# Performance work log

Hardware: AMD Instinct MI355X
Metric: run time of the kernel (lower is better)

## Reference

```python
import jax, jax.numpy as jnp
import numpy as np

OUT_F, IN_F = 4096, 4096
GROUP = 128
NGROUPS = IN_F // GROUP  # 32


def setup_inputs() -> dict:
    key = jax.random.key(0)
    k1, k2, k3, k4 = jax.random.split(key, 4)
    x = jax.random.normal(k1, (4, 2048, IN_F), dtype=jnp.float32)
    # 4-bit codes stored as integers in [0, 16)
    compressed_weight = jax.random.randint(k2, (OUT_F, IN_F), 0, 16, dtype=jnp.int32)
    scale = jax.random.uniform(k3, (OUT_F, NGROUPS), dtype=jnp.float32)
    offset = jax.random.normal(k4, (OUT_F, NGROUPS), dtype=jnp.float32)
    return {"x": x, "compressed_weight": compressed_weight, "scale": scale, "offset": offset}


def reference(x, compressed_weight, scale, offset):
    # group-wise dequant: w[o, g, j] = code * scale[o, g] - offset[o, g]
    codes = compressed_weight.astype(scale.dtype).reshape(OUT_F, NGROUPS, GROUP)
    w = (codes * scale[..., None] - offset[..., None]).reshape(OUT_F, IN_F)
    # F.linear: x @ w.T  -> [B, S, OUT_F]
    return jnp.einsum('bsi,oi->bso', x, w.astype(x.dtype))
```

## Files before the change

### kernel.cpp

```cpp
#include <hip/hip_runtime.h>
#include <stdint.h>

#define OUT_F 4096
#define IN_F  4096
#define NGROUPS 32
#define BK 64
#define NT (IN_F / BK)

typedef __attribute__((ext_vector_type(4)))  float    f32x4;
typedef __attribute__((ext_vector_type(8)))  short    bf16x8;
typedef __attribute__((ext_vector_type(4)))  int      i32x4;
typedef __attribute__((ext_vector_type(4)))  uint32_t u32x4;

__device__ __forceinline__ ushort f2bf(float f) {
  union { float f; uint32_t u; } v; v.f = f;
  uint32_t r = v.u + 0x7FFFu + ((v.u >> 16) & 1u);
  return (ushort)(r >> 16);
}

__global__ void cvt_x_kernel(const float* __restrict__ x, ushort* __restrict__ xb, int n8) {
  int i = blockIdx.x * blockDim.x + threadIdx.x;
  if (i >= n8) return;
  const f32x4* xp = (const f32x4*)x;
  f32x4 a = xp[2 * i], b = xp[2 * i + 1];
  u32x4 o;
  o.x = (uint32_t)f2bf(a.x) | ((uint32_t)f2bf(a.y) << 16);
  o.y = (uint32_t)f2bf(a.z) | ((uint32_t)f2bf(a.w) << 16);
  o.z = (uint32_t)f2bf(b.x) | ((uint32_t)f2bf(b.y) << 16);
  o.w = (uint32_t)f2bf(b.z) | ((uint32_t)f2bf(b.w) << 16);
  ((u32x4*)xb)[i] = o;
}

__global__ void dequant_w_kernel(const int* __restrict__ cw,
                                 const float* __restrict__ sc,
                                 const float* __restrict__ of,
                                 ushort* __restrict__ wb) {
  int t = blockIdx.x * blockDim.x + threadIdx.x;
  int o  = t >> 9;
  int k0 = (t & 511) << 3;
  int g  = k0 >> 7;
  float s   = sc[o * NGROUPS + g];
  float off = of[o * NGROUPS + g];
  const i32x4* cp = (const i32x4*)(cw + (size_t)o * IN_F + k0);
  i32x4 c0 = cp[0], c1 = cp[1];
  u32x4 out;
  out.x = (uint32_t)f2bf((float)c0.x * s - off) | ((uint32_t)f2bf((float)c0.y * s - off) << 16);
  out.y = (uint32_t)f2bf((float)c0.z * s - off) | ((uint32_t)f2bf((float)c0.w * s - off) << 16);
  out.z = (uint32_t)f2bf((float)c1.x * s - off) | ((uint32_t)f2bf((float)c1.y * s - off) << 16);
  out.w = (uint32_t)f2bf((float)c1.z * s - off) | ((uint32_t)f2bf((float)c1.w * s - off) << 16);
  *(u32x4*)(wb + (size_t)o * IN_F + k0) = out;
}


#define BAR() do { asm volatile("" ::: "memory"); __builtin_amdgcn_s_barrier(); asm volatile("" ::: "memory"); } while (0)

#define GLLDS(gp, lp) __builtin_amdgcn_global_load_lds( \
  (const __attribute__((address_space(1))) uint32_t*)(const void*)(gp), \
  (__attribute__((address_space(3))) uint32_t*)(void*)(lp), 16, 0, 0)

#define STAGE_A(buf, kt) do { \
  _Pragma("unroll") for (int q_ = 0; q_ < 4; ++q_) \
    GLLDS(A + (size_t)(m0 + q_ * 64 + stRow) * IN_F + (kt) * BK + sl * 8, \
          ldsb + (buf) * 65536 + q_ * 8192 + wid * 1024); \
} while (0)

#define STAGE_B(buf, kt) do { \
  _Pragma("unroll") for (int q_ = 0; q_ < 4; ++q_) \
    GLLDS(B + (size_t)(n0 + q_ * 64 + stRow) * IN_F + (kt) * BK + sl * 8, \
          ldsb + (buf) * 65536 + 32768 + q_ * 8192 + wid * 1024); \
} while (0)

#define RD_AH(dst, i0, base, H, OFF) do { \
  _Pragma("unroll") for (int i_ = 0; i_ < 4; ++i_) \
    dst[i_][H] = *(const bf16x8*)((base) + ((i0) + i_) * 2048 + (OFF)); \
} while (0)

#define RD_BH(dst, j0, base, H, OFF) do { \
  _Pragma("unroll") for (int j_ = 0; j_ < 2; ++j_) \
    dst[j_][H] = *(const bf16x8*)((base) + ((j0) + j_) * 2048 + (OFF)); \
} while (0)

#define MFMAH(I0, J0, Aset, Bset, H) do { \
  __builtin_amdgcn_s_setprio(1); \
  _Pragma("unroll") for (int i_ = 0; i_ < 4; ++i_) \
  _Pragma("unroll") for (int j_ = 0; j_ < 2; ++j_) \
    acc[(I0) + i_][(J0) + j_] = __builtin_amdgcn_mfma_f32_16x16x32_bf16(Aset[i_][H], Bset[j_][H], acc[(I0) + i_][(J0) + j_], 0, 0, 0); \
  __builtin_amdgcn_s_setprio(0); \
} while (0)

__global__ __launch_bounds__(512, 2) void gemm256(const ushort* __restrict__ A,
                                                  const ushort* __restrict__ B,
                                                  float* __restrict__ C, int M) {
  __shared__ ushort lds[65536];
  char* ldsb = (char*)lds;

  const int nmt = M >> 8;
  const int nwg = gridDim.x;
  int wg = blockIdx.x;
  if ((nwg & 7) == 0) wg = (wg & 7) * (nwg >> 3) + (wg >> 3);
  const int bn = wg / nmt;
  const int bm = wg % nmt;
  const int m0 = bm << 8, n0 = bn << 8;

  const int tid  = threadIdx.x;
  const int lane = tid & 63;
  const int wid  = tid >> 6;
  const int wr   = wid >> 2;
  const int wc   = wid & 3;

  const int stRow = wid * 8 + (lane >> 3);
  const int sl    = (lane & 7) ^ (lane >> 3);

  const int frow = lane & 15;
  const int g    = lane >> 4;
  const int off0 = frow * 128 + (((g    ) ^ (lane & 7)) << 4);
  const int off1 = frow * 128 + (((4 + g) ^ (lane & 7)) << 4);

  f32x4 acc[8][4] = {};
  bf16x8 A0_[4][2], A1_[4][2], B0_[2][2], B1_[2][2];

  STAGE_A(0, 0); STAGE_B(0, 0);
  STAGE_A(1, 1); STAGE_B(1, 1);
  asm volatile("s_waitcnt vmcnt(8)" ::: "memory");
  BAR();
  RD_AH(A0_, 0, ldsb + wr * 16384, 0, off0);
  RD_BH(B0_, 0, ldsb + 32768 + wc * 8192, 0, off0);

#pragma unroll 1
  for (int t = 0; t < NT; ++t) {
    const int cur = t & 1, nxt = cur ^ 1;
    const char* aC = ldsb + cur * 65536 + wr * 16384;
    const char* bC = ldsb + cur * 65536 + 32768 + wc * 8192;
    const char* aN = ldsb + nxt * 65536 + wr * 16384;
    const char* bN = ldsb + nxt * 65536 + 32768 + wc * 8192;

    RD_BH(B1_, 2, bC, 0, off0);
    RD_AH(A1_, 4, aC, 0, off0);
    MFMAH(0, 0, A0_, B0_, 0);

    RD_AH(A0_, 0, aC, 1, off1);
    MFMAH(0, 2, A0_, B1_, 0);

    RD_BH(B0_, 0, bC, 1, off1);
    MFMAH(4, 0, A1_, B0_, 0);

    RD_BH(B1_, 2, bC, 1, off1);
    RD_AH(A1_, 4, aC, 1, off1);
    MFMAH(4, 2, A1_, B1_, 0);

    MFMAH(0, 0, A0_, B0_, 1);
    asm volatile("s_waitcnt lgkmcnt(0)" ::: "memory");
    if (t + 1 < NT) { asm volatile("s_waitcnt vmcnt(4)" ::: "memory"); }
    BAR();

    if (t + 1 < NT) RD_AH(A0_, 0, aN, 0, off0);
    if (t + 2 < NT) STAGE_A(cur, t + 2);
    MFMAH(0, 2, A0_, B1_, 1);
    if (t + 2 < NT)      { asm volatile("s_waitcnt vmcnt(4)" ::: "memory"); }
    else if (t + 1 < NT) { asm volatile("s_waitcnt vmcnt(0)" ::: "memory"); }
    BAR();

    if (t + 1 < NT) RD_BH(B0_, 0, bN, 0, off0);
    if (t + 2 < NT) STAGE_B(cur, t + 2);
    MFMAH(4, 0, A1_, B0_, 1);

    MFMAH(4, 2, A1_, B1_, 1);
  }

  const int crow0 = m0 + wr * 128 + (g << 2);
  const int ccol0 = n0 + wc * 64 + frow;
#pragma unroll
  for (int mf = 0; mf < 8; ++mf)
#pragma unroll
    for (int nf = 0; nf < 4; ++nf)
#pragma unroll
      for (int q = 0; q < 4; ++q)
        C[(size_t)(crow0 + mf * 16 + q) * OUT_F + (ccol0 + nf * 16)] = acc[mf][nf][q];
}

__global__ void naive_kernel(const float* __restrict__ x, const int* __restrict__ cw,
                             const float* __restrict__ sc, const float* __restrict__ of,
                             float* __restrict__ out, int M) {
  int idx = blockIdx.x * blockDim.x + threadIdx.x;
  if (idx >= M * OUT_F) return;
  int o = idx & (OUT_F - 1);
  int m = idx >> 12;
  const float* xr = x + (size_t)m * IN_F;
  const int*   wr = cw + (size_t)o * IN_F;
  float acc = 0.f;
  for (int gg = 0; gg < NGROUPS; ++gg) {
    float s = sc[o * NGROUPS + gg], off = of[o * NGROUPS + gg];
#pragma unroll 8
    for (int k = 0; k < 128; ++k) {
      int kk = (gg << 7) + k;
      acc += xr[kk] * ((float)wr[kk] * s - off);
    }
  }
  out[idx] = acc;
}

extern "C" void kernel_launch(void* const* d_in, const int* in_sizes, int n_in,
                              void* d_out, int out_size, void* d_ws, size_t ws_size,
                              hipStream_t stream) {
  const float* x  = (const float*)d_in[0];
  const int*   cw = (const int*)d_in[1];
  const float* sc = (const float*)d_in[2];
  const float* of = (const float*)d_in[3];
  float* out = (float*)d_out;
  const int M = in_sizes[0] / IN_F;

  const size_t xb_bytes = (size_t)M * IN_F * 2;
  const size_t wb_bytes = (size_t)OUT_F * IN_F * 2;

  if (ws_size >= xb_bytes + wb_bytes && (M % 256) == 0) {
    ushort* xb = (ushort*)d_ws;
    ushort* wb = (ushort*)((char*)d_ws + xb_bytes);

    int n8 = (M * IN_F) / 8;
    cvt_x_kernel<<<(n8 + 255) / 256, 256, 0, stream>>>(x, xb, n8);

    int nw8 = (OUT_F * IN_F) / 8;
    dequant_w_kernel<<<(nw8 + 255) / 256, 256, 0, stream>>>(cw, sc, of, wb);

    dim3 grid((M / 256) * (OUT_F / 256));
    gemm256<<<grid, 512, 0, stream>>>(xb, wb, out, M);
  } else {
    int total = M * OUT_F;
    naive_kernel<<<(total + 255) / 256, 256, 0, stream>>>(x, cw, sc, of, out, M);
  }
}
```

Before: 286.8 us.

## Restructure GEMM main loop into barrier-separated quadrant phases

Replaces the software-pipelined main loop with four quadrant phases. The old loop prefetched the next tile's fragments into registers across iterations and interleaved half-K MFMA groups. Each new phase loads a full-K A or B fragment set from LDS, runs 16 MFMAs on one output quadrant, and is bracketed by workgroup barriers. Global-to-LDS staging of the next tiles is moved between phases, with adjusted vmcnt waits. This simplifies the schedule and may line up memory and MFMA phases across the waves on a CU, but it drops the cross-iteration register prefetch and adds many barriers per K-step, which risks exposed LDS latency.

New measurement: 302.5 us. 1.05x slower.

```diff
diff --git a/kernel.cpp b/kernel.cpp
--- a/kernel.cpp
+++ b/kernel.cpp
@@ -80,11 +80,12 @@
     dst[j_][H] = *(const bf16x8*)((base) + ((j0) + j_) * 2048 + (OFF)); \
 } while (0)
 
-#define MFMAH(I0, J0, Aset, Bset, H) do { \
+#define MFMAQ16(I0, J0, Aset, Bset) do { \
   __builtin_amdgcn_s_setprio(1); \
+  _Pragma("unroll") for (int h_ = 0; h_ < 2; ++h_) \
   _Pragma("unroll") for (int i_ = 0; i_ < 4; ++i_) \
   _Pragma("unroll") for (int j_ = 0; j_ < 2; ++j_) \
-    acc[(I0) + i_][(J0) + j_] = __builtin_amdgcn_mfma_f32_16x16x32_bf16(Aset[i_][H], Bset[j_][H], acc[(I0) + i_][(J0) + j_], 0, 0, 0); \
+    acc[(I0) + i_][(J0) + j_] = __builtin_amdgcn_mfma_f32_16x16x32_bf16(Aset[i_][h_], Bset[j_][h_], acc[(I0) + i_][(J0) + j_], 0, 0, 0); \
   __builtin_amdgcn_s_setprio(0); \
 } while (0)
 
@@ -117,54 +118,45 @@
   const int off1 = frow * 128 + (((4 + g) ^ (lane & 7)) << 4);
 
   f32x4 acc[8][4] = {};
-  bf16x8 A0_[4][2], A1_[4][2], B0_[2][2], B1_[2][2];
+  bf16x8 Al[4][2], Ah[4][2], Bl[2][2], Bh[2][2];
 
   STAGE_A(0, 0); STAGE_B(0, 0);
   STAGE_A(1, 1); STAGE_B(1, 1);
   asm volatile("s_waitcnt vmcnt(8)" ::: "memory");
   BAR();
-  RD_AH(A0_, 0, ldsb + wr * 16384, 0, off0);
-  RD_BH(B0_, 0, ldsb + 32768 + wc * 8192, 0, off0);
 
 #pragma unroll 1
   for (int t = 0; t < NT; ++t) {
-    const int cur = t & 1, nxt = cur ^ 1;
+    const int cur = t & 1;
     const char* aC = ldsb + cur * 65536 + wr * 16384;
     const char* bC = ldsb + cur * 65536 + 32768 + wc * 8192;
-    const char* aN = ldsb + nxt * 65536 + wr * 16384;
-    const char* bN = ldsb + nxt * 65536 + 32768 + wc * 8192;
-
-    RD_BH(B1_, 2, bC, 0, off0);
-    RD_AH(A1_, 4, aC, 0, off0);
-    MFMAH(0, 0, A0_, B0_, 0);
-
-    RD_AH(A0_, 0, aC, 1, off1);
-    MFMAH(0, 2, A0_, B1_, 0);
-
-    RD_BH(B0_, 0, bC, 1, off1);
-    MFMAH(4, 0, A1_, B0_, 0);
-
-    RD_BH(B1_, 2, bC, 1, off1);
-    RD_AH(A1_, 4, aC, 1, off1);
-    MFMAH(4, 2, A1_, B1_, 0);
-
-    MFMAH(0, 0, A0_, B0_, 1);
-    asm volatile("s_waitcnt lgkmcnt(0)" ::: "memory");
-    if (t + 1 < NT) { asm volatile("s_waitcnt vmcnt(4)" ::: "memory"); }
-    BAR();
-
-    if (t + 1 < NT) RD_AH(A0_, 0, aN, 0, off0);
-    if (t + 2 < NT) STAGE_A(cur, t + 2);
-    MFMAH(0, 2, A0_, B1_, 1);
-    if (t + 2 < NT)      { asm volatile("s_waitcnt vmcnt(4)" ::: "memory"); }
-    else if (t + 1 < NT) { asm volatile("s_waitcnt vmcnt(0)" ::: "memory"); }
-    BAR();
-
-    if (t + 1 < NT) RD_BH(B0_, 0, bN, 0, off0);
+
+    RD_AH(Al, 0, aC, 0, off0); RD_AH(Al, 0, aC, 1, off1);
+    RD_BH(Bl, 0, bC, 0, off0); RD_BH(Bl, 0, bC, 1, off1);
+    BAR();
+    MFMAQ16(0, 0, Al, Bl);
+    BAR();
+
+    RD_BH(Bh, 2, bC, 0, off0); RD_BH(Bh, 2, bC, 1, off1);
+    BAR();
+    MFMAQ16(0, 2, Al, Bh);
+    BAR();
+
+    RD_AH(Ah, 4, aC, 0, off0); RD_AH(Ah, 4, aC, 1, off1);
     if (t + 2 < NT) STAGE_B(cur, t + 2);
-    MFMAH(4, 0, A1_, B0_, 1);
-
-    MFMAH(4, 2, A1_, B1_, 1);
+    BAR();
+    MFMAQ16(4, 2, Ah, Bh);
+    BAR();
+
+    if (t + 2 < NT) {
+      STAGE_A(cur, t + 2);
+      asm volatile("s_waitcnt vmcnt(8)" ::: "memory");
+    } else if (t + 1 < NT) {
+      asm volatile("s_waitcnt vmcnt(0)" ::: "memory");
+    }
+    BAR();
+    MFMAQ16(4, 0, Ah, Bl);
+    BAR();
   }
 
   const int crow0 = m0 + wr * 128 + (g << 2);
```
